# Kernel tuning notes

Measured on AMD Instinct MI355X. Metric: run time of the kernel, lower is better.

## Reference

```python
import jax, jax.numpy as jnp
import numpy as np
import math

D_MODEL = 1024
NUM_HEADS = 16
HEAD_DIM = D_MODEL // NUM_HEADS


def setup_inputs() -> dict:
    key = jax.random.key(0)
    ks = jax.random.split(key, 10)
    B, Sq, Skv = 2, 2048, 2048
    s = 1.0 / math.sqrt(D_MODEL)
    return {
        "X": jax.random.normal(ks[0], (B, Skv, D_MODEL), jnp.float32),
        "y": jax.random.normal(ks[1], (B, Sq, D_MODEL), jnp.float32),
        "qW": jax.random.normal(ks[2], (D_MODEL, D_MODEL), jnp.float32) * s,
        "qB": jnp.zeros((D_MODEL,), jnp.float32),
        "kW": jax.random.normal(ks[3], (D_MODEL, D_MODEL), jnp.float32) * s,
        "kB": jnp.zeros((D_MODEL,), jnp.float32),
        "vW": jax.random.normal(ks[4], (D_MODEL, D_MODEL), jnp.float32) * s,
        "vB": jnp.zeros((D_MODEL,), jnp.float32),
        "oW": jax.random.normal(ks[5], (D_MODEL, D_MODEL), jnp.float32) * s,
        "oB": jnp.zeros((D_MODEL,), jnp.float32),
    }


def _split_heads(x):
    # (B, S, D) -> (B, H, S, dk)
    B, S, _ = x.shape
    return x.reshape(B, S, NUM_HEADS, HEAD_DIM).transpose(0, 2, 1, 3)


def reference(X, y, qW, qB, kW, kB, vW, vB, oW, oB):
    B = X.shape[0]
    q = _split_heads(y @ qW + qB)   # queries come from y (decoder)
    k = _split_heads(X @ kW + kB)   # keys/values from X (encoder)
    v = _split_heads(X @ vW + vB)
    scale = 1.0 / math.sqrt(HEAD_DIM)
    scores = jnp.einsum("bhqd,bhkd->bhqk", q, k) * scale
    weights = jax.nn.softmax(scores, axis=-1)
    attn = jnp.einsum("bhqk,bhkd->bhqd", weights, v)
    concat = attn.transpose(0, 2, 1, 3).reshape(B, -1, D_MODEL)
    return concat @ oW + oB
```

## Files before the change

kernel.cpp:

```cpp
#include <hip/hip_runtime.h>
#include <hip/hip_bf16.h>
#include <math.h>

typedef __hip_bfloat16 bf16;
typedef __bf16 nbf16;
typedef __bf16 bf16x8 __attribute__((ext_vector_type(8)));
typedef __bf16 bf16x4 __attribute__((ext_vector_type(4)));
typedef float f32x4 __attribute__((ext_vector_type(4)));

#define D_MODEL 1024
#define NHEAD   16
#define HDK     64
#define BATCH   2
#define SEQ     2048
#define QSZ     ((size_t)BATCH * SEQ * D_MODEL)
#define WSZ     ((size_t)D_MODEL * D_MODEL)

__global__ void detect_dtype(const unsigned short* __restrict__ x, int* flag) {
    __shared__ int cnt;
    if (threadIdx.x == 0) cnt = 0;
    __syncthreads();
    int local = 0;
    for (int i = threadIdx.x; i < 4096; i += 256) {
        const unsigned short v = x[i];
        const int e = (v >> 7) & 0xFF;
        if (v == 0 || (e >= 96 && e <= 141)) local++;
    }
    atomicAdd(&cnt, local);
    __syncthreads();
    if (threadIdx.x == 0) *flag = (cnt >= 3600) ? 1 : 0;
}

__device__ __forceinline__ float ldIn(const void* p, size_t i, int isbf16) {
    return isbf16 ? __bfloat162float(((const bf16*)p)[i])
                  : ((const float*)p)[i];
}

__device__ __forceinline__ void gload_lds16(const void* g, void* l) {
    __builtin_amdgcn_global_load_lds(
        (const __attribute__((address_space(1))) void*)g,
        (__attribute__((address_space(3))) void*)l, 16, 0, 0);
}

__global__ void tobf16(const void* __restrict__ in, nbf16* __restrict__ out,
                       const int* __restrict__ flagp) {
    const int flag = *flagp;
    const size_t i = ((size_t)blockIdx.x * 256 + threadIdx.x) * 8;
    if (flag) {
        *(uint4*)(out + i) = *(const uint4*)((const nbf16*)in + i);
    } else {
        const float4 a = *(const float4*)((const float*)in + i);
        const float4 b = *(const float4*)((const float*)in + i + 4);
        bf16x8 v = {(nbf16)a.x, (nbf16)a.y, (nbf16)a.z, (nbf16)a.w,
                    (nbf16)b.x, (nbf16)b.y, (nbf16)b.z, (nbf16)b.w};
        *(bf16x8*)(out + i) = v;
    }
}

__global__ void wtrans(const void* __restrict__ W, nbf16* __restrict__ Wt,
                       const int* __restrict__ flagp) {
    const int flag = *flagp;
    __shared__ float T[64][65];
    const int k0 = blockIdx.x * 64, n0 = blockIdx.y * 64;
    #pragma unroll
    for (int i = 0; i < 16; ++i) {
        const int idx = threadIdx.x + i * 256;
        const int r = idx >> 6, c = idx & 63;
        T[r][c] = ldIn(W, (size_t)(k0 + r) * D_MODEL + n0 + c, flag);
    }
    __syncthreads();
    #pragma unroll
    for (int i = 0; i < 16; ++i) {
        const int idx = threadIdx.x + i * 256;
        const int n = idx >> 6, k = idx & 63;
        Wt[(size_t)(n0 + n) * D_MODEL + k0 + k] = (nbf16)T[k][n];
    }
}

#define STAGE128(Albuf, Blbuf, Aptr, Bptr, t)                                  \
{                                                                              \
    const int _k0 = (t) * 64;                                                  \
    _Pragma("unroll")                                                          \
    for (int i = 0; i < 4; ++i) {                                              \
        const int row = i * 32 + wid * 8 + (lane >> 3);                        \
        const int ss  = (lane & 7) ^ (row & 7);                                \
        gload_lds16((Aptr) + (size_t)row * D_MODEL + _k0 + ss * 8,             \
                    (nbf16*)(Albuf) + i * 2048 + wid * 512);                   \
        gload_lds16((Bptr) + (size_t)row * D_MODEL + _k0 + ss * 8,             \
                    (nbf16*)(Blbuf) + i * 2048 + wid * 512);                   \
    }                                                                          \
}

#define GEMM128_LOOP(Al, Bl)                                                   \
    const int NT = D_MODEL / 64;                                               \
    for (int t = 0; t < NT; ++t) {                                             \
        const int cur = t & 1;                                                 \
        if (t + 1 < NT)                                                        \
            STAGE128(&Al[cur ^ 1][0][0], &Bl[cur ^ 1][0][0], Am, Bm, t + 1);   \
        _Pragma("unroll")                                                      \
        for (int kk = 0; kk < 2; ++kk) {                                       \
            bf16x8 af[4], bfr[4];                                              \
            _Pragma("unroll")                                                  \
            for (int mi = 0; mi < 4; ++mi) {                                   \
                const int ar = wr * 64 + mi * 16 + l15;                        \
                const int sl = ((kk << 2) + lg) ^ (ar & 7);                    \
                af[mi] = *(const bf16x8*)((const nbf16*)&Al[cur][ar][0] + sl * 8); \
            }                                                                  \
            _Pragma("unroll")                                                  \
            for (int ni = 0; ni < 4; ++ni) {                                   \
                const int br = wc * 64 + ni * 16 + l15;                        \
                const int sl = ((kk << 2) + lg) ^ (br & 7);                    \
                bfr[ni] = *(const bf16x8*)((const nbf16*)&Bl[cur][br][0] + sl * 8); \
            }                                                                  \
            _Pragma("unroll")                                                  \
            for (int mi = 0; mi < 4; ++mi)                                     \
                _Pragma("unroll")                                              \
                for (int ni = 0; ni < 4; ++ni)                                 \
                    acc[mi][ni] = __builtin_amdgcn_mfma_f32_16x16x32_bf16(     \
                        af[mi], bfr[ni], acc[mi][ni], 0, 0, 0);                \
        }                                                                      \
        __syncthreads();                                                       \
    }

__global__ __launch_bounds__(256, 2) void proj_qkv(
        const nbf16* __restrict__ Xb, const nbf16* __restrict__ Yb,
        const nbf16* __restrict__ Wt3,
        const void* __restrict__ qB, const void* __restrict__ kB,
        const void* __restrict__ vB,
        nbf16* __restrict__ outq, const int* __restrict__ flagp) {
    __shared__ nbf16 Al[2][128][64];
    __shared__ nbf16 Bl[2][128][64];

    const int flag = *flagp;
    const int tid  = threadIdx.x;
    const int wid  = tid >> 6;
    const int lane = tid & 63;
    const int l15  = lane & 15;
    const int lg   = lane >> 4;
    const int wr   = wid >> 1;
    const int wc   = wid & 1;

    const int id = blockIdx.x;
    const int sw = (id & 7) * 96 + (id >> 3);
    const int m0  = (sw & 31) * 128;
    const int ng0 = (sw >> 5) * 128;

    const nbf16* A  = (ng0 < D_MODEL) ? Yb : Xb;
    const nbf16* Bm = Wt3 + (size_t)ng0 * D_MODEL;
    const nbf16* Am = A + (size_t)m0 * D_MODEL;

    f32x4 acc[4][4];
    #pragma unroll
    for (int mi = 0; mi < 4; ++mi)
        #pragma unroll
        for (int ni = 0; ni < 4; ++ni) acc[mi][ni] = (f32x4){0.f, 0.f, 0.f, 0.f};

    STAGE128(&Al[0][0][0], &Bl[0][0][0], Am, Bm, 0);
    __syncthreads();

    GEMM128_LOOP(Al, Bl)

    #pragma unroll
    for (int ni = 0; ni < 4; ++ni) {
        const int n  = ng0 + wc * 64 + ni * 16 + l15;
        const int wh = n >> 10;
        const int nl = n & 1023;
        const void* bp = (wh == 0) ? qB : (wh == 1) ? kB : vB;
        const float bias = ldIn(bp, (size_t)nl, flag);
        nbf16* outp = outq + (size_t)wh * QSZ;
        #pragma unroll
        for (int mi = 0; mi < 4; ++mi) {
            #pragma unroll
            for (int r = 0; r < 4; ++r) {
                const int m = m0 + wr * 64 + mi * 16 + lg * 4 + r;
                const float v = acc[mi][ni][r] + bias;
                const int b = m >> 11, s = m & (SEQ - 1);
                const int h = nl >> 6,  d = nl & (HDK - 1);
                outp[(((size_t)(b * NHEAD + h)) * SEQ + s) * HDK + d] = (nbf16)v;
            }
        }
    }
}

__global__ __launch_bounds__(256, 2) void proj_o(
        const nbf16* __restrict__ A, const nbf16* __restrict__ Wt,
        const void* __restrict__ Braw, void* __restrict__ Cout,
        const int* __restrict__ flagp) {
    __shared__ nbf16 Al[2][128][64];
    __shared__ nbf16 Bl[2][128][64];

    const int flag = *flagp;
    const int tid  = threadIdx.x;
    const int wid  = tid >> 6;
    const int lane = tid & 63;
    const int l15  = lane & 15;
    const int lg   = lane >> 4;
    const int wr   = wid >> 1;
    const int wc   = wid & 1;

    const int id = blockIdx.x;
    const int sw = (id & 7) * 32 + (id >> 3);
    const int m0 = (sw >> 3) * 128;
    const int n0 = (sw & 7) * 128;

    const nbf16* Am = A + (size_t)m0 * D_MODEL;
    const nbf16* Bm = Wt + (size_t)n0 * D_MODEL;

    f32x4 acc[4][4];
    #pragma unroll
    for (int mi = 0; mi < 4; ++mi)
        #pragma unroll
        for (int ni = 0; ni < 4; ++ni) acc[mi][ni] = (f32x4){0.f, 0.f, 0.f, 0.f};

    STAGE128(&Al[0][0][0], &Bl[0][0][0], Am, Bm, 0);
    __syncthreads();

    GEMM128_LOOP(Al, Bl)

    #pragma unroll
    for (int ni = 0; ni < 4; ++ni) {
        const int n = n0 + wc * 64 + ni * 16 + l15;
        const float bias = ldIn(Braw, (size_t)n, flag);
        #pragma unroll
        for (int mi = 0; mi < 4; ++mi) {
            #pragma unroll
            for (int r = 0; r < 4; ++r) {
                const int m = m0 + wr * 64 + mi * 16 + lg * 4 + r;
                const float v = acc[mi][ni][r] + bias;
                if (flag) ((bf16*)Cout)[(size_t)m * D_MODEL + n] = __float2bfloat16(v);
                else      ((float*)Cout)[(size_t)m * D_MODEL + n] = v;
            }
        }
    }
}

__global__ __launch_bounds__(256, 2) void attn_mfma(
        const nbf16* __restrict__ qg, const nbf16* __restrict__ kg,
        const nbf16* __restrict__ vg, nbf16* __restrict__ cg) {
    __shared__ nbf16 KL[2][64][64];
    __shared__ nbf16 VT[2][64][72];
    __shared__ nbf16 PB[4][32][72];

    const int tid  = threadIdx.x;
    const int wid  = tid >> 6;
    const int lane = tid & 63;
    const int l15  = lane & 15;
    const int lg   = lane >> 4;

    const int id = blockIdx.x;
    const int sw = (id & 7) * 64 + (id >> 3);
    const int bh = sw >> 4;
    const int qt = sw & 15;

    const nbf16* qb = qg + (size_t)bh * SEQ * HDK;
    const nbf16* kb = kg + (size_t)bh * SEQ * HDK;
    const nbf16* vb = vg + (size_t)bh * SEQ * HDK;

    const int qbase = qt * 128 + wid * 32;
    const nbf16* qpA = qb + (size_t)(qbase + l15) * HDK + lg * 8;
    const nbf16* qpB = qpA + 16 * HDK;
    const bf16x8 qfA0 = *(const bf16x8*)qpA;
    const bf16x8 qfA1 = *(const bf16x8*)(qpA + 32);
    const bf16x8 qfB0 = *(const bf16x8*)qpB;
    const bf16x8 qfB1 = *(const bf16x8*)(qpB + 32);

    const int g8 = (tid >> 5) * 8;
    const int p2 = (tid & 31) * 2;

    #define STAGEK(buf, t)                                                     \
    {                                                                          \
        _Pragma("unroll")                                                      \
        for (int i = 0; i < 2; ++i) {                                          \
            const int row = i * 32 + wid * 8 + (lane >> 3);                    \
            const int ss  = (lane & 7) ^ (row & 7);                            \
            gload_lds16(kb + (size_t)((t) * 64 + row) * HDK + ss * 8,          \
                        (nbf16*)&KL[buf][0][0] + i * 2048 + wid * 512);        \
        }                                                                      \
    }

    #define VLOAD(t)                                                           \
        a0 = *(const uint4*)(vb + (size_t)((t) * 64 + p2) * HDK + g8);         \
        a1 = *(const uint4*)(vb + (size_t)((t) * 64 + p2 + 1) * HDK + g8);

    #define VWRITE(buf)                                                        \
    {                                                                          \
        const unsigned short* e0 = (const unsigned short*)&a0;                 \
        const unsigned short* e1 = (const unsigned short*)&a1;                 \
        _Pragma("unroll")                                                      \
        for (int j = 0; j < 8; ++j)                                            \
            *(unsigned int*)&VT[buf][g8 + j][p2] =                             \
                (unsigned int)e0[j] | ((unsigned int)e1[j] << 16);             \
    }

    const float SC = 0.125f * 1.44269504088896340736f;

    #define SOFTMAX(st, m2, lden, o, pbrow)                                    \
    do {                                                                       \
        float tm = -3.0e38f;                                                   \
        _Pragma("unroll")                                                      \
        for (int s_ = 0; s_ < 4; ++s_)                                         \
            _Pragma("unroll")                                                  \
            for (int r = 0; r < 4; ++r) {                                      \
                st[s_][r] *= SC;                                               \
                tm = fmaxf(tm, st[s_][r]);                                     \
            }                                                                  \
        tm = fmaxf(tm, __shfl_xor(tm, 16, 64));                                \
        tm = fmaxf(tm, __shfl_xor(tm, 32, 64));                                \
        const bool nresc = __all(tm - m2 <= 8.0f);                             \
        const float mref = nresc ? m2 : fmaxf(m2, tm);                         \
        float ts = 0.f;                                                        \
        _Pragma("unroll")                                                      \
        for (int s_ = 0; s_ < 4; ++s_) {                                       \
            const float p0 = exp2f(st[s_][0] - mref);                          \
            const float p1 = exp2f(st[s_][1] - mref);                          \
            const float p2_ = exp2f(st[s_][2] - mref);                         \
            const float p3 = exp2f(st[s_][3] - mref);                          \
            ts += (p0 + p1) + (p2_ + p3);                                      \
            bf16x4 pk = {(nbf16)p0, (nbf16)p1, (nbf16)p2_, (nbf16)p3};         \
            *(bf16x4*)((pbrow) + s_ * 16 + lg * 4) = pk;                       \
        }                                                                      \
        ts += __shfl_xor(ts, 16, 64);                                          \
        ts += __shfl_xor(ts, 32, 64);                                          \
        if (nresc) {                                                           \
            lden += ts;                                                        \
        } else {                                                               \
            const float alpha = exp2f(m2 - mref);                              \
            lden = lden * alpha + ts;                                          \
            m2 = mref;                                                         \
            float av[4];                                                       \
            _Pragma("unroll")                                                  \
            for (int r = 0; r < 4; ++r) av[r] = __shfl(alpha, lg * 4 + r, 64); \
            _Pragma("unroll")                                                  \
            for (int i = 0; i < 4; ++i)                                        \
                _Pragma("unroll")                                              \
                for (int r = 0; r < 4; ++r) o[i][r] *= av[r];                  \
        }                                                                      \
    } while (0)

    float m2A = -3.0e38f, ldenA = 0.f;
    float m2B = -3.0e38f, ldenB = 0.f;
    f32x4 oA[4], oB[4];
    #pragma unroll
    for (int i = 0; i < 4; ++i) { oA[i] = (f32x4){0,0,0,0}; oB[i] = (f32x4){0,0,0,0}; }

    const int NT = SEQ / 64;

    {
        uint4 a0, a1;
        STAGEK(0, 0);
        VLOAD(0);
        VWRITE(0);
    }
    __syncthreads();

    for (int t = 0; t < NT; ++t) {
        const int cur = t & 1;
        uint4 a0, a1;
        if (t + 1 < NT) {
            STAGEK(cur ^ 1, t + 1);
            VLOAD(t + 1);
        }

        f32x4 stA[4], stB[4];
        __builtin_amdgcn_s_setprio(1);
        #pragma unroll
        for (int sub = 0; sub < 4; ++sub) {
            const int row = sub * 16 + l15;
            const int s0 = lg ^ (row & 7);
            const int s1 = (4 + lg) ^ (row & 7);
            const bf16x8 kf0 = *(const bf16x8*)((const nbf16*)&KL[cur][row][0] + s0 * 8);
            const bf16x8 kf1 = *(const bf16x8*)((const nbf16*)&KL[cur][row][0] + s1 * 8);
            f32x4 a = (f32x4){0,0,0,0};
            a = __builtin_amdgcn_mfma_f32_16x16x32_bf16(kf0, qfA0, a, 0, 0, 0);
            a = __builtin_amdgcn_mfma_f32_16x16x32_bf16(kf1, qfA1, a, 0, 0, 0);
            stA[sub] = a;
            f32x4 b = (f32x4){0,0,0,0};
            b = __builtin_amdgcn_mfma_f32_16x16x32_bf16(kf0, qfB0, b, 0, 0, 0);
            b = __builtin_amdgcn_mfma_f32_16x16x32_bf16(kf1, qfB1, b, 0, 0, 0);
            stB[sub] = b;
        }
        __builtin_amdgcn_s_setprio(0);

        SOFTMAX(stA, m2A, ldenA, oA, &PB[wid][l15][0]);
        SOFTMAX(stB, m2B, ldenB, oB, &PB[wid][16 + l15][0]);

        __asm__ volatile("s_waitcnt lgkmcnt(0)" ::: "memory");

        const bf16x8 pfA0 = *(const bf16x8*)&PB[wid][l15][lg * 8];
        const bf16x8 pfA1 = *(const bf16x8*)&PB[wid][l15][lg * 8 + 32];
        const bf16x8 pfB0 = *(const bf16x8*)&PB[wid][16 + l15][lg * 8];
        const bf16x8 pfB1 = *(const bf16x8*)&PB[wid][16 + l15][lg * 8 + 32];
        __builtin_amdgcn_s_setprio(1);
        #pragma unroll
        for (int db = 0; db < 4; ++db) {
            const bf16x8 vf0 = *(const bf16x8*)&VT[cur][db * 16 + l15][lg * 8];
            const bf16x8 vf1 = *(const bf16x8*)&VT[cur][db * 16 + l15][lg * 8 + 32];
            oA[db] = __builtin_amdgcn_mfma_f32_16x16x32_bf16(pfA0, vf0, oA[db], 0, 0, 0);
            oA[db] = __builtin_amdgcn_mfma_f32_16x16x32_bf16(pfA1, vf1, oA[db], 0, 0, 0);
            oB[db] = __builtin_amdgcn_mfma_f32_16x16x32_bf16(pfB0, vf0, oB[db], 0, 0, 0);
            oB[db] = __builtin_amdgcn_mfma_f32_16x16x32_bf16(pfB1, vf1, oB[db], 0, 0, 0);
        }
        __builtin_amdgcn_s_setprio(0);

        if (t + 1 < NT) VWRITE(cur ^ 1);
        __syncthreads();
    }

    const int b = bh >> 4, h = bh & 15;
    float invdA[4], invdB[4];
    #pragma unroll
    for (int r = 0; r < 4; ++r) {
        invdA[r] = 1.f / __shfl(ldenA, lg * 4 + r, 64);
        invdB[r] = 1.f / __shfl(ldenB, lg * 4 + r, 64);
    }
    #pragma unroll
    for (int db = 0; db < 4; ++db) {
        #pragma unroll
        for (int r = 0; r < 4; ++r) {
            const int qA = qbase + lg * 4 + r;
            cg[((size_t)(b * SEQ + qA)) * D_MODEL + h * HDK + db * 16 + l15] =
                (nbf16)(oA[db][r] * invdA[r]);
            const int qB_ = qbase + 16 + lg * 4 + r;
            cg[((size_t)(b * SEQ + qB_)) * D_MODEL + h * HDK + db * 16 + l15] =
                (nbf16)(oB[db][r] * invdB[r]);
        }
    }
    #undef STAGEK
    #undef VLOAD
    #undef VWRITE
    #undef SOFTMAX
}

extern "C" void kernel_launch(void* const* d_in, const int* in_sizes, int n_in,
                              void* d_out, int out_size, void* d_ws, size_t ws_size,
                              hipStream_t stream) {
    const void* X  = d_in[0];
    const void* Y  = d_in[1];
    const void* qW = d_in[2];
    const void* qB = d_in[3];
    const void* kW = d_in[4];
    const void* kB = d_in[5];
    const void* vW = d_in[6];
    const void* vB = d_in[7];
    const void* oW = d_in[8];
    const void* oB = d_in[9];

    nbf16* ws = (nbf16*)d_ws;
    nbf16* qbuf = ws;
    nbf16* kbuf = qbuf + QSZ;
    nbf16* vbuf = kbuf + QSZ;
    nbf16* cbuf = vbuf + QSZ;
    nbf16* Xb   = cbuf + QSZ;
    nbf16* Yb   = Xb + QSZ;
    nbf16* Wt3  = Yb + QSZ;
    nbf16* Wto  = Wt3 + 3 * WSZ;
    int*   flag = (int*)(Wto + WSZ);

    detect_dtype<<<1, 256, 0, stream>>>((const unsigned short*)X, flag);

    tobf16<<<(int)(QSZ / (256 * 8)), 256, 0, stream>>>(X, Xb, flag);
    tobf16<<<(int)(QSZ / (256 * 8)), 256, 0, stream>>>(Y, Yb, flag);

    const dim3 tg(16, 16);
    wtrans<<<tg, 256, 0, stream>>>(qW, Wt3, flag);
    wtrans<<<tg, 256, 0, stream>>>(kW, Wt3 + WSZ, flag);
    wtrans<<<tg, 256, 0, stream>>>(vW, Wt3 + 2 * WSZ, flag);
    wtrans<<<tg, 256, 0, stream>>>(oW, Wto, flag);

    proj_qkv<<<768, 256, 0, stream>>>(Xb, Yb, Wt3, qB, kB, vB, qbuf, flag);

    attn_mfma<<<512, 256, 0, stream>>>(qbuf, kbuf, vbuf, cbuf);

    proj_o<<<256, 256, 0, stream>>>(cbuf, Wto, oB, d_out, flag);
}
```

Baseline: 278.6 us.

## Shrink attention tiles, read K from global directly, and merge prep launches

The attention kernel now gives each block 64 queries instead of 128, so each wave handles 16 query rows instead of 32. The grid doubles to 1024 blocks and the launch bound rises to 4 blocks per SM, aiming at higher occupancy from fewer registers and less LDS. K tiles are no longer staged into LDS with async loads. Each wave reads its K fragments straight from global memory, which removes the KL buffer but exposes global latency inside the QK loop and halves K reuse per load. Separately, the two dtype-conversion launches and the four weight-transpose launches are merged into single launches, and the softmax row max becomes a tree reduction.

```diff
diff --git a/kernel.cpp b/kernel.cpp
--- a/kernel.cpp
+++ b/kernel.cpp
@@ -42,10 +42,16 @@
         (__attribute__((address_space(3))) void*)l, 16, 0, 0);
 }
 
-__global__ void tobf16(const void* __restrict__ in, nbf16* __restrict__ out,
-                       const int* __restrict__ flagp) {
+__global__ void tobf16_xy(const void* __restrict__ X, const void* __restrict__ Y,
+                          nbf16* __restrict__ Xb, nbf16* __restrict__ Yb,
+                          const int* __restrict__ flagp) {
     const int flag = *flagp;
-    const size_t i = ((size_t)blockIdx.x * 256 + threadIdx.x) * 8;
+    const int half = (int)(QSZ / 2048);
+    const bool isX = blockIdx.x < half;
+    const void* in = isX ? X : Y;
+    nbf16* out     = isX ? Xb : Yb;
+    const size_t i = ((size_t)(isX ? blockIdx.x : blockIdx.x - half) * 256 +
+                      threadIdx.x) * 8;
     if (flag) {
         *(uint4*)(out + i) = *(const uint4*)((const nbf16*)in + i);
     } else {
@@ -57,9 +63,15 @@
     }
 }
 
-__global__ void wtrans(const void* __restrict__ W, nbf16* __restrict__ Wt,
-                       const int* __restrict__ flagp) {
+__global__ void wtrans4(const void* __restrict__ qW, const void* __restrict__ kW,
+                        const void* __restrict__ vW, const void* __restrict__ oW,
+                        nbf16* __restrict__ Wt3, nbf16* __restrict__ Wto,
+                        const int* __restrict__ flagp) {
     const int flag = *flagp;
+    const int z = blockIdx.z;
+    const void* W = (z == 0) ? qW : (z == 1) ? kW : (z == 2) ? vW : oW;
+    nbf16* Wt = (z == 3) ? Wto : Wt3 + (size_t)z * WSZ;
+
     __shared__ float T[64][65];
     const int k0 = blockIdx.x * 64, n0 = blockIdx.y * 64;
     #pragma unroll
@@ -234,12 +246,11 @@
     }
 }
 
-__global__ __launch_bounds__(256, 2) void attn_mfma(
+__global__ __launch_bounds__(256, 4) void attn_mfma(
         const nbf16* __restrict__ qg, const nbf16* __restrict__ kg,
         const nbf16* __restrict__ vg, nbf16* __restrict__ cg) {
-    __shared__ nbf16 KL[2][64][64];
     __shared__ nbf16 VT[2][64][72];
-    __shared__ nbf16 PB[4][32][72];
+    __shared__ nbf16 PB[4][16][72];
 
     const int tid  = threadIdx.x;
     const int wid  = tid >> 6;
@@ -248,35 +259,21 @@
     const int lg   = lane >> 4;
 
     const int id = blockIdx.x;
-    const int sw = (id & 7) * 64 + (id >> 3);
-    const int bh = sw >> 4;
-    const int qt = sw & 15;
+    const int sw = (id & 7) * 128 + (id >> 3);
+    const int bh = sw >> 5;
+    const int qt = sw & 31;
 
     const nbf16* qb = qg + (size_t)bh * SEQ * HDK;
     const nbf16* kb = kg + (size_t)bh * SEQ * HDK;
     const nbf16* vb = vg + (size_t)bh * SEQ * HDK;
 
-    const int qbase = qt * 128 + wid * 32;
-    const nbf16* qpA = qb + (size_t)(qbase + l15) * HDK + lg * 8;
-    const nbf16* qpB = qpA + 16 * HDK;
-    const bf16x8 qfA0 = *(const bf16x8*)qpA;
-    const bf16x8 qfA1 = *(const bf16x8*)(qpA + 32);
-    const bf16x8 qfB0 = *(const bf16x8*)qpB;
-    const bf16x8 qfB1 = *(const bf16x8*)(qpB + 32);
+    const int qbase = qt * 64 + wid * 16;
+    const nbf16* qp = qb + (size_t)(qbase + l15) * HDK + lg * 8;
+    const bf16x8 qf0 = *(const bf16x8*)qp;
+    const bf16x8 qf1 = *(const bf16x8*)(qp + 32);
 
     const int g8 = (tid >> 5) * 8;
     const int p2 = (tid & 31) * 2;
-
-    #define STAGEK(buf, t)                                                     \
-    {                                                                          \
-        _Pragma("unroll")                                                      \
-        for (int i = 0; i < 2; ++i) {                                          \
-            const int row = i * 32 + wid * 8 + (lane >> 3);                    \
-            const int ss  = (lane & 7) ^ (row & 7);                            \
-            gload_lds16(kb + (size_t)((t) * 64 + row) * HDK + ss * 8,          \
-                        (nbf16*)&KL[buf][0][0] + i * 2048 + wid * 512);        \
-        }                                                                      \
-    }
 
     #define VLOAD(t)                                                           \
         a0 = *(const uint4*)(vb + (size_t)((t) * 64 + p2) * HDK + g8);         \
@@ -296,14 +293,16 @@
 
     #define SOFTMAX(st, m2, lden, o, pbrow)                                    \
     do {                                                                       \
-        float tm = -3.0e38f;                                                   \
         _Pragma("unroll")                                                      \
         for (int s_ = 0; s_ < 4; ++s_)                                         \
             _Pragma("unroll")                                                  \
-            for (int r = 0; r < 4; ++r) {                                      \
-                st[s_][r] *= SC;                                               \
-                tm = fmaxf(tm, st[s_][r]);                                     \
-            }                                                                  \
+            for (int r = 0; r < 4; ++r) st[s_][r] *= SC;                       \
+        float tmx[4];                                                          \
+        _Pragma("unroll")                                                      \
+        for (int s_ = 0; s_ < 4; ++s_)                                         \
+            tmx[s_] = fmaxf(fmaxf(st[s_][0], st[s_][1]),                       \
+                            fmaxf(st[s_][2], st[s_][3]));                      \
+        float tm = fmaxf(fmaxf(tmx[0], tmx[1]), fmaxf(tmx[2], tmx[3]));        \
         tm = fmaxf(tm, __shfl_xor(tm, 16, 64));                                \
         tm = fmaxf(tm, __shfl_xor(tm, 32, 64));                                \
         const bool nresc = __all(tm - m2 <= 8.0f);                             \
@@ -337,17 +336,15 @@
         }                                                                      \
     } while (0)
 
-    float m2A = -3.0e38f, ldenA = 0.f;
-    float m2B = -3.0e38f, ldenB = 0.f;
-    f32x4 oA[4], oB[4];
-    #pragma unroll
-    for (int i = 0; i < 4; ++i) { oA[i] = (f32x4){0,0,0,0}; oB[i] = (f32x4){0,0,0,0}; }
+    float m2 = -3.0e38f, lden = 0.f;
+    f32x4 o[4];
+    #pragma unroll
+    for (int i = 0; i < 4; ++i) o[i] = (f32x4){0, 0, 0, 0};
 
     const int NT = SEQ / 64;
 
     {
         uint4 a0, a1;
-        STAGEK(0, 0);
         VLOAD(0);
         VWRITE(0);
     }
@@ -356,49 +353,36 @@
     for (int t = 0; t < NT; ++t) {
         const int cur = t & 1;
         uint4 a0, a1;
-        if (t + 1 < NT) {
-            STAGEK(cur ^ 1, t + 1);
-            VLOAD(t + 1);
-        }
-
-        f32x4 stA[4], stB[4];
+        if (t + 1 < NT) VLOAD(t + 1);
+
+        f32x4 st[4];
+        const nbf16* kt = kb + (size_t)t * 64 * HDK;
         __builtin_amdgcn_s_setprio(1);
         #pragma unroll
         for (int sub = 0; sub < 4; ++sub) {
-            const int row = sub * 16 + l15;
-            const int s0 = lg ^ (row & 7);
-            const int s1 = (4 + lg) ^ (row & 7);
-            const bf16x8 kf0 = *(const bf16x8*)((const nbf16*)&KL[cur][row][0] + s0 * 8);
-            const bf16x8 kf1 = *(const bf16x8*)((const nbf16*)&KL[cur][row][0] + s1 * 8);
-            f32x4 a = (f32x4){0,0,0,0};
-            a = __builtin_amdgcn_mfma_f32_16x16x32_bf16(kf0, qfA0, a, 0, 0, 0);
-            a = __builtin_amdgcn_mfma_f32_16x16x32_bf16(kf1, qfA1, a, 0, 0, 0);
-            stA[sub] = a;
-            f32x4 b = (f32x4){0,0,0,0};
-            b = __builtin_amdgcn_mfma_f32_16x16x32_bf16(kf0, qfB0, b, 0, 0, 0);
-            b = __builtin_amdgcn_mfma_f32_16x16x32_bf16(kf1, qfB1, b, 0, 0, 0);
-            stB[sub] = b;
+            const nbf16* kp = kt + (size_t)(sub * 16 + l15) * HDK + lg * 8;
+            const bf16x8 kf0 = *(const bf16x8*)kp;
+            const bf16x8 kf1 = *(const bf16x8*)(kp + 32);
+            f32x4 a = (f32x4){0, 0, 0, 0};
+            a = __builtin_amdgcn_mfma_f32_16x16x32_bf16(kf0, qf0, a, 0, 0, 0);
+            a = __builtin_amdgcn_mfma_f32_16x16x32_bf16(kf1, qf1, a, 0, 0, 0);
+            st[sub] = a;
         }
         __builtin_amdgcn_s_setprio(0);
 
-        SOFTMAX(stA, m2A, ldenA, oA, &PB[wid][l15][0]);
-        SOFTMAX(stB, m2B, ldenB, oB, &PB[wid][16 + l15][0]);
+        SOFTMAX(st, m2, lden, o, &PB[wid][l15][0]);
 
         __asm__ volatile("s_waitcnt lgkmcnt(0)" ::: "memory");
 
-        const bf16x8 pfA0 = *(const bf16x8*)&PB[wid][l15][lg * 8];
-        const bf16x8 pfA1 = *(const bf16x8*)&PB[wid][l15][lg * 8 + 32];
-        const bf16x8 pfB0 = *(const bf16x8*)&PB[wid][16 + l15][lg * 8];
-        const bf16x8 pfB1 = *(const bf16x8*)&PB[wid][16 + l15][lg * 8 + 32];
+        const bf16x8 pf0 = *(const bf16x8*)&PB[wid][l15][lg * 8];
+        const bf16x8 pf1 = *(const bf16x8*)&PB[wid][l15][lg * 8 + 32];
         __builtin_amdgcn_s_setprio(1);
         #pragma unroll
         for (int db = 0; db < 4; ++db) {
             const bf16x8 vf0 = *(const bf16x8*)&VT[cur][db * 16 + l15][lg * 8];
             const bf16x8 vf1 = *(const bf16x8*)&VT[cur][db * 16 + l15][lg * 8 + 32];
-            oA[db] = __builtin_amdgcn_mfma_f32_16x16x32_bf16(pfA0, vf0, oA[db], 0, 0, 0);
-            oA[db] = __builtin_amdgcn_mfma_f32_16x16x32_bf16(pfA1, vf1, oA[db], 0, 0, 0);
-            oB[db] = __builtin_amdgcn_mfma_f32_16x16x32_bf16(pfB0, vf0, oB[db], 0, 0, 0);
-            oB[db] = __builtin_amdgcn_mfma_f32_16x16x32_bf16(pfB1, vf1, oB[db], 0, 0, 0);
+            o[db] = __builtin_amdgcn_mfma_f32_16x16x32_bf16(pf0, vf0, o[db], 0, 0, 0);
+            o[db] = __builtin_amdgcn_mfma_f32_16x16x32_bf16(pf1, vf1, o[db], 0, 0, 0);
         }
         __builtin_amdgcn_s_setprio(0);
 
@@ -407,25 +391,19 @@
     }
 
     const int b = bh >> 4, h = bh & 15;
-    float invdA[4], invdB[4];
-    #pragma unroll
-    for (int r = 0; r < 4; ++r) {
-        invdA[r] = 1.f / __shfl(ldenA, lg * 4 + r, 64);
-        invdB[r] = 1.f / __shfl(ldenB, lg * 4 + r, 64);
-    }
+    float invd[4];
+    #pragma unroll
+    for (int r = 0; r < 4; ++r)
+        invd[r] = 1.f / __shfl(lden, lg * 4 + r, 64);
     #pragma unroll
     for (int db = 0; db < 4; ++db) {
         #pragma unroll
         for (int r = 0; r < 4; ++r) {
-            const int qA = qbase + lg * 4 + r;
-            cg[((size_t)(b * SEQ + qA)) * D_MODEL + h * HDK + db * 16 + l15] =
-                (nbf16)(oA[db][r] * invdA[r]);
-            const int qB_ = qbase + 16 + lg * 4 + r;
-            cg[((size_t)(b * SEQ + qB_)) * D_MODEL + h * HDK + db * 16 + l15] =
-                (nbf16)(oB[db][r] * invdB[r]);
+            const int qr2 = qbase + lg * 4 + r;
+            cg[((size_t)(b * SEQ + qr2)) * D_MODEL + h * HDK + db * 16 + l15] =
+                (nbf16)(o[db][r] * invd[r]);
         }
     }
-    #undef STAGEK
     #undef VLOAD
     #undef VWRITE
     #undef SOFTMAX
@@ -458,18 +436,13 @@
 
     detect_dtype<<<1, 256, 0, stream>>>((const unsigned short*)X, flag);
 
-    tobf16<<<(int)(QSZ / (256 * 8)), 256, 0, stream>>>(X, Xb, flag);
-    tobf16<<<(int)(QSZ / (256 * 8)), 256, 0, stream>>>(Y, Yb, flag);
-
-    const dim3 tg(16, 16);
-    wtrans<<<tg, 256, 0, stream>>>(qW, Wt3, flag);
-    wtrans<<<tg, 256, 0, stream>>>(kW, Wt3 + WSZ, flag);
-    wtrans<<<tg, 256, 0, stream>>>(vW, Wt3 + 2 * WSZ, flag);
-    wtrans<<<tg, 256, 0, stream>>>(oW, Wto, flag);
+    tobf16_xy<<<(int)(2 * (QSZ / 2048)), 256, 0, stream>>>(X, Y, Xb, Yb, flag);
+
+    wtrans4<<<dim3(16, 16, 4), 256, 0, stream>>>(qW, kW, vW, oW, Wt3, Wto, flag);
 
     proj_qkv<<<768, 256, 0, stream>>>(Xb, Yb, Wt3, qB, kB, vB, qbuf, flag);
 
-    attn_mfma<<<512, 256, 0, stream>>>(qbuf, kbuf, vbuf, cbuf);
+    attn_mfma<<<1024, 256, 0, stream>>>(qbuf, kbuf, vbuf, cbuf);
 
     proj_o<<<256, 256, 0, stream>>>(cbuf, Wto, oB, d_out, flag);
 }
```

Result: slower. 325.6 us (+16.9%).
